# Performance work log

Measured on AMD Instinct MI355X. Metric: run time of the kernel, lower is better.

Reference implementation:

```python
import jax, jax.numpy as jnp
import numpy as np

B, S, D = 2, 2048, 1024
H, DK = 16, 64  # n_heads, d_kv; inner_dim = H*DK = D


def setup_inputs() -> dict:
    key = jax.random.key(0)
    ks = jax.random.split(key, 7)
    scale = 1.0 / np.sqrt(D)
    return {
        "hidden_states": jax.random.normal(ks[0], (B, S, D), dtype=jnp.float32),
        "position_bias": jax.random.normal(ks[1], (1, H, S, S), dtype=jnp.float32) * 0.1,
        "key_value_states": jax.random.normal(ks[2], (B, S, D), dtype=jnp.float32),
        "wq": jax.random.normal(ks[3], (D, H * DK), dtype=jnp.float32) * scale,
        "wk": jax.random.normal(ks[4], (D, H * DK), dtype=jnp.float32) * scale,
        "wv": jax.random.normal(ks[5], (D, H * DK), dtype=jnp.float32) * scale,
        "wo": jax.random.normal(ks[6], (H * DK, D), dtype=jnp.float32) * scale,
    }


def reference(hidden_states, position_bias, key_value_states, wq, wk, wv, wo):
    # Self-attention branch (is_cross_attention=False): K/V come from hidden_states.
    b, s, _ = hidden_states.shape
    kv_src = hidden_states  # would be key_value_states if cross-attention

    def split_heads(x):  # [b, s, H*DK] -> [b, H, s, DK]
        return x.reshape(b, -1, H, DK).transpose(0, 2, 1, 3)

    q = split_heads(hidden_states @ wq)
    k = split_heads(kv_src @ wk)
    v = split_heads(kv_src @ wv)

    # T5-style: NO 1/sqrt(d_k) scaling; additive position bias.
    scores = jnp.einsum("bhqd,bhkd->bhqk", q, k) + position_bias
    attn = jax.nn.softmax(scores.astype(jnp.float32), axis=-1).astype(scores.dtype)
    ctx = jnp.einsum("bhqk,bhkd->bhqd", attn, v)
    ctx = ctx.transpose(0, 2, 1, 3).reshape(b, s, H * DK)
    return ctx @ wo
```

## Files before the change

kernel.cpp:

```cpp
#include <hip/hip_runtime.h>
#include <math.h>

#define B_  2
#define S_  2048
#define D_  1024
#define H_  16
#define DK_ 64

typedef float f32x4 __attribute__((ext_vector_type(4)));
typedef short short8 __attribute__((ext_vector_type(8)));
typedef unsigned short u16;

static __device__ __forceinline__ u16 f2bf(float x) {
    union { float f; unsigned u; } v; v.f = x;
    unsigned r = v.u + 0x7fffu + ((v.u >> 16) & 1u);
    return (u16)(r >> 16);
}

static __device__ __forceinline__ void gload_lds16(const void* g, void* l) {
    __builtin_amdgcn_global_load_lds((const __attribute__((address_space(1))) void*)g,
                                     (__attribute__((address_space(3))) void*)l,
                                     16, 0, 0);
}

#define MFMA16(a, b, c) __builtin_amdgcn_mfma_f32_16x16x32_bf16((a), (b), (c), 0, 0, 0)

__global__ __launch_bounds__(256) void cast_bf16(const float* __restrict__ X,
                                                 u16* __restrict__ Y) {
    int i = (blockIdx.x * 256 + threadIdx.x) * 8;
    float4 a = *(const float4*)(X + i);
    float4 b = *(const float4*)(X + i + 4);
    short8 o;
    o[0] = (short)f2bf(a.x); o[1] = (short)f2bf(a.y);
    o[2] = (short)f2bf(a.z); o[3] = (short)f2bf(a.w);
    o[4] = (short)f2bf(b.x); o[5] = (short)f2bf(b.y);
    o[6] = (short)f2bf(b.z); o[7] = (short)f2bf(b.w);
    *(short8*)(Y + i) = o;
}

__global__ __launch_bounds__(256) void transpose_cast4(const float* __restrict__ w0,
                                                       const float* __restrict__ w1,
                                                       const float* __restrict__ w2,
                                                       const float* __restrict__ w3,
                                                       u16* __restrict__ o0,
                                                       u16* __restrict__ o1,
                                                       u16* __restrict__ o2,
                                                       u16* __restrict__ o3) {
    __shared__ float t[32][33];
    const float* W; u16* O;
    switch (blockIdx.z) {
        case 0: W = w0; O = o0; break;
        case 1: W = w1; O = o1; break;
        case 2: W = w2; O = o2; break;
        default: W = w3; O = o3; break;
    }
    const int K = 1024, N = 1024;
    int tx = threadIdx.x & 31, ty = threadIdx.x >> 5;
    int n0 = blockIdx.x * 32, k0 = blockIdx.y * 32;
#pragma unroll
    for (int r = ty; r < 32; r += 8)
        t[r][tx] = W[(size_t)(k0 + r) * N + n0 + tx];
    __syncthreads();
#pragma unroll
    for (int r = ty; r < 32; r += 8)
        O[(size_t)(n0 + r) * K + k0 + tx] = f2bf(t[tx][r]);
}

template <int MODE>
__global__ __launch_bounds__(256) void gemm_bf16(const u16* __restrict__ A,
                                                 const u16* __restrict__ Bt,
                                                 void* __restrict__ C0,
                                                 u16* __restrict__ Kb,
                                                 u16* __restrict__ Vt,
                                                 int M, int N, int K) {
    __shared__ alignas(16) u16 As[128 * 32];
    __shared__ alignas(16) u16 Bs[128 * 32];

    const int tid  = threadIdx.x;
    const int wave = tid >> 6;
    const int lane = tid & 63;
    const int col  = lane & 15;
    const int quad = lane >> 4;
    const int bm   = blockIdx.y * 128;
    const int bn   = blockIdx.x * 128;
    const int wm   = (wave >> 1) * 64;
    const int wn   = (wave & 1) * 64;

    f32x4 acc[4][4];
#pragma unroll
    for (int i = 0; i < 4; ++i)
#pragma unroll
        for (int j = 0; j < 4; ++j) acc[i][j] = (f32x4){0.f, 0.f, 0.f, 0.f};

    const int srow = wave * 32 + (lane >> 2);
    const int ksel = (lane & 3) * 8;
    const u16* ga0 = A  + (size_t)(bm + srow) * K + ksel;
    const u16* ga1 = ga0 + (size_t)16 * K;
    const u16* gb0 = Bt + (size_t)(bn + srow) * K + ksel;
    const u16* gb1 = gb0 + (size_t)16 * K;
    char* la0 = (char*)As + wave * 2048;
    char* la1 = la0 + 1024;
    char* lb0 = (char*)Bs + wave * 2048;
    char* lb1 = lb0 + 1024;

    for (int k0 = 0; k0 < K; k0 += 32) {
        __syncthreads();
        gload_lds16(ga0 + k0, la0);
        gload_lds16(ga1 + k0, la1);
        gload_lds16(gb0 + k0, lb0);
        gload_lds16(gb1 + k0, lb1);
        __syncthreads();
        short8 af[4], bfr[4];
#pragma unroll
        for (int mi = 0; mi < 4; ++mi)
            af[mi] = *(const short8*)&As[(wm + mi * 16 + col) * 32 + quad * 8];
#pragma unroll
        for (int ni = 0; ni < 4; ++ni)
            bfr[ni] = *(const short8*)&Bs[(wn + ni * 16 + col) * 32 + quad * 8];
#pragma unroll
        for (int mi = 0; mi < 4; ++mi)
#pragma unroll
            for (int ni = 0; ni < 4; ++ni)
                acc[mi][ni] = MFMA16(af[mi], bfr[ni], acc[mi][ni]);
    }

#pragma unroll
    for (int mi = 0; mi < 4; ++mi)
#pragma unroll
        for (int ni = 0; ni < 4; ++ni) {
            const int rowb = bm + wm + mi * 16 + quad * 4;
            const int coln = bn + wn + ni * 16 + col;
            f32x4 v = acc[mi][ni];
            if (MODE == 2) {
                float* O = (float*)C0;
#pragma unroll
                for (int r = 0; r < 4; ++r)
                    O[(size_t)(rowb + r) * N + coln] = v[r];
            } else {
                if (coln < D_) {
                    u16* Qb = (u16*)C0;
#pragma unroll
                    for (int r = 0; r < 4; ++r)
                        Qb[(size_t)(rowb + r) * D_ + coln] = f2bf(v[r]);
                } else if (coln < 2 * D_) {
#pragma unroll
                    for (int r = 0; r < 4; ++r)
                        Kb[(size_t)(rowb + r) * D_ + (coln - D_)] = f2bf(v[r]);
                } else {
                    const int nn = coln - 2 * D_;
                    const int hh = nn >> 6, d = nn & 63;
                    const int bb = rowb >> 11, sb = rowb & 2047;
                    ushort4 pk;
                    pk.x = f2bf(v[0]); pk.y = f2bf(v[1]);
                    pk.z = f2bf(v[2]); pk.w = f2bf(v[3]);
                    *(ushort4*)&Vt[(((size_t)bb * H_ + hh) * DK_ + d) * S_ + sb] = pk;
                }
            }
        }
}

__global__ __launch_bounds__(256, 4) void attn_mfma(const u16* __restrict__ Qb,
                                                    const u16* __restrict__ Kb,
                                                    const u16* __restrict__ Vt,
                                                    const float* __restrict__ bias,
                                                    u16* __restrict__ Ctx) {
    __shared__ alignas(16) char smem[40960];

    const int tid  = threadIdx.x;
    const int wave = tid >> 6;
    const int lane = tid & 63;
    const int col  = lane & 15;
    const int quad = lane >> 4;
    const int cx   = col & 7;
    const int sl0  = (quad ^ cx) * 16;
    const int sl1  = ((4 + quad) ^ cx) * 16;

    const int gid = blockIdx.x;
    const int qt  = gid & 31;
    const int h   = (gid >> 5) & 15;
    const int b   = gid >> 9;
    const int q0  = qt * 64 + wave * 16;

    short8 aq0, aq1;
    {
        const u16* qp = Qb + (size_t)(b * S_ + q0 + col) * D_ + h * 64 + quad * 8;
        aq0 = *(const short8*)qp;
        aq1 = *(const short8*)(qp + 32);
    }

    const int c0 = tid, c1 = tid + 256;
    const int r0 = c0 >> 3, g0 = (c0 & 7) ^ (r0 & 7);
    const int r1 = c1 >> 3, g1 = (c1 & 7) ^ (r1 & 7);
    const u16* kT = Kb + (size_t)b * S_ * D_ + h * 64;
    const u16* vT = Vt + ((size_t)b * H_ + h) * (size_t)64 * S_;
    const size_t kOff0 = (size_t)r0 * D_ + g0 * 8;
    const size_t kOff1 = (size_t)r1 * D_ + g1 * 8;
    const size_t vOff0 = (size_t)r0 * S_ + g0 * 8;
    const size_t vOff1 = (size_t)r1 * S_ + g1 * 8;

    auto stage = [&](int j0s, int bis) {
        char* base = smem + bis * 16384;
        gload_lds16(kT + (size_t)j0s * D_ + kOff0, base + wave * 1024);
        gload_lds16(kT + (size_t)j0s * D_ + kOff1, base + 4096 + wave * 1024);
        gload_lds16(vT + j0s + vOff0, base + 8192 + wave * 1024);
        gload_lds16(vT + j0s + vOff1, base + 12288 + wave * 1024);
    };

    f32x4 o[4];
#pragma unroll
    for (int i = 0; i < 4; ++i) o[i] = (f32x4){0.f, 0.f, 0.f, 0.f};
    float mst[4], lst[4];
#pragma unroll
    for (int r = 0; r < 4; ++r) { mst[r] = -INFINITY; lst[r] = 0.f; }

    const float* bias_base = bias + ((size_t)h * S_ + (q0 + quad * 4)) * S_;
    char* pw = smem + 32768 + wave * 2048;

    stage(0, 0);

    for (int it = 0; it < 32; ++it) {
        const int j0 = it * 64;
        const int bi = it & 1;
        __syncthreads();
        if (it < 31) stage(j0 + 64, bi ^ 1);

        const char* bK = smem + bi * 16384;
        const char* bV = bK + 8192;

        float bb[16];
#pragma unroll
        for (int ng = 0; ng < 4; ++ng)
#pragma unroll
            for (int r = 0; r < 4; ++r)
                bb[ng * 4 + r] = bias_base[(size_t)r * S_ + j0 + ng * 16 + col];

        f32x4 sc[4];
#pragma unroll
        for (int ng = 0; ng < 4; ++ng) {
            const char* rp = bK + (ng * 16 + col) * 128;
            short8 k0 = *(const short8*)(rp + sl0);
            short8 k1 = *(const short8*)(rp + sl1);
            f32x4 z = (f32x4){0.f, 0.f, 0.f, 0.f};
            z = MFMA16(aq0, k0, z);
            z = MFMA16(aq1, k1, z);
            sc[ng] = z;
        }
#pragma unroll
        for (int ng = 0; ng < 4; ++ng)
#pragma unroll
            for (int r = 0; r < 4; ++r) sc[ng][r] += bb[ng * 4 + r];

        float alpha[4], rs[4];
#pragma unroll
        for (int r = 0; r < 4; ++r) {
            float rm = fmaxf(fmaxf(sc[0][r], sc[1][r]), fmaxf(sc[2][r], sc[3][r]));
            rm = fmaxf(rm, __shfl_xor(rm, 1));
            rm = fmaxf(rm, __shfl_xor(rm, 2));
            rm = fmaxf(rm, __shfl_xor(rm, 4));
            rm = fmaxf(rm, __shfl_xor(rm, 8));
            float mn = fmaxf(mst[r], rm);
            alpha[r] = __expf(mst[r] - mn);
            mst[r] = mn;
            rs[r] = 0.f;
        }
#pragma unroll
        for (int ng = 0; ng < 4; ++ng)
#pragma unroll
            for (int r = 0; r < 4; ++r) {
                float p = __expf(sc[ng][r] - mst[r]);
                sc[ng][r] = p;
                rs[r] += p;
            }
#pragma unroll
        for (int r = 0; r < 4; ++r) {
            float s = rs[r];
            s += __shfl_xor(s, 1);
            s += __shfl_xor(s, 2);
            s += __shfl_xor(s, 4);
            s += __shfl_xor(s, 8);
            lst[r] = lst[r] * alpha[r] + s;
        }
#pragma unroll
        for (int ndg = 0; ndg < 4; ++ndg)
#pragma unroll
            for (int r = 0; r < 4; ++r) o[ndg][r] *= alpha[r];

#pragma unroll
        for (int ng = 0; ng < 4; ++ng) {
            const int cb = ng * 2 + (col >> 3);
#pragma unroll
            for (int r = 0; r < 4; ++r) {
                const int q = quad * 4 + r;
                *(u16*)(pw + q * 128 + ((cb ^ (q & 7)) * 16) + cx * 2) = f2bf(sc[ng][r]);
            }
        }
        short8 ap0 = *(const short8*)(pw + col * 128 + sl0);
        short8 ap1 = *(const short8*)(pw + col * 128 + sl1);

#pragma unroll
        for (int ndg = 0; ndg < 4; ++ndg) {
            const char* rp = bV + (ndg * 16 + col) * 128;
            short8 v0 = *(const short8*)(rp + sl0);
            short8 v1 = *(const short8*)(rp + sl1);
            o[ndg] = MFMA16(ap0, v0, o[ndg]);
            o[ndg] = MFMA16(ap1, v1, o[ndg]);
        }
    }

    float inv[4];
#pragma unroll
    for (int r = 0; r < 4; ++r) inv[r] = 1.f / lst[r];
#pragma unroll
    for (int ndg = 0; ndg < 4; ++ndg)
#pragma unroll
        for (int r = 0; r < 4; ++r)
            Ctx[(size_t)(b * S_ + q0 + quad * 4 + r) * D_ + h * 64 + ndg * 16 + col] =
                f2bf(o[ndg][r] * inv[r]);
}

extern "C" void kernel_launch(void* const* d_in, const int* in_sizes, int n_in,
                              void* d_out, int out_size, void* d_ws, size_t ws_size,
                              hipStream_t stream) {
    const float* hs   = (const float*)d_in[0];
    const float* bias = (const float*)d_in[1];
    const float* wq   = (const float*)d_in[3];
    const float* wk   = (const float*)d_in[4];
    const float* wv   = (const float*)d_in[5];
    const float* wo   = (const float*)d_in[6];
    float* out = (float*)d_out;

    const size_t elems = (size_t)B_ * S_ * D_;
    char* ws = (char*)d_ws;
    u16* hs_bf = (u16*)ws;
    u16* qb    = (u16*)(ws + 8 * 1024 * 1024);
    u16* kb    = (u16*)(ws + 16 * 1024 * 1024);
    u16* vt    = (u16*)(ws + 24 * 1024 * 1024);
    u16* cb    = (u16*)(ws + 32 * 1024 * 1024);
    u16* wqt   = (u16*)(ws + 40 * 1024 * 1024);
    u16* wkt   = (u16*)(ws + 42 * 1024 * 1024);
    u16* wvt   = (u16*)(ws + 44 * 1024 * 1024);
    u16* wot   = (u16*)(ws + 46 * 1024 * 1024);

    const int M = B_ * S_;

    cast_bf16<<<(int)(elems / (256 * 8)), 256, 0, stream>>>(hs, hs_bf);
    transpose_cast4<<<dim3(32, 32, 4), 256, 0, stream>>>(wq, wk, wv, wo,
                                                         wqt, wkt, wvt, wot);

    gemm_bf16<0><<<dim3(3 * D_ / 128, M / 128), 256, 0, stream>>>(
        hs_bf, wqt, (void*)qb, kb, vt, M, 3 * D_, D_);

    attn_mfma<<<B_ * H_ * (S_ / 64), 256, 0, stream>>>(qb, kb, vt, bias, cb);

    gemm_bf16<2><<<dim3(D_ / 128, M / 128), 256, 0, stream>>>(
        cb, wot, (void*)out, nullptr, nullptr, M, D_, D_);
}
```

Measured before the change: 528.6 us.

## Double-buffer GEMM LDS tiles and merge cast and transpose prep kernels

The bf16 GEMM now keeps two LDS buffers for A and B. The next k-slice's global-to-LDS load is issued right after the barrier, while the current slice feeds the MFMAs, and the second barrier per iteration is gone. It also adds a launch-bounds occupancy hint of 2. Separately, the hidden-state cast and the weight transpose-cast are merged into one launch, using an extra grid z-slice, to save a kernel launch. The cost is doubled LDS use per block, which could limit occupancy.

```diff
diff --git a/kernel.cpp b/kernel.cpp
--- a/kernel.cpp
+++ b/kernel.cpp
@@ -25,27 +25,31 @@
 
 #define MFMA16(a, b, c) __builtin_amdgcn_mfma_f32_16x16x32_bf16((a), (b), (c), 0, 0, 0)
 
-__global__ __launch_bounds__(256) void cast_bf16(const float* __restrict__ X,
-                                                 u16* __restrict__ Y) {
-    int i = (blockIdx.x * 256 + threadIdx.x) * 8;
-    float4 a = *(const float4*)(X + i);
-    float4 b = *(const float4*)(X + i + 4);
-    short8 o;
-    o[0] = (short)f2bf(a.x); o[1] = (short)f2bf(a.y);
-    o[2] = (short)f2bf(a.z); o[3] = (short)f2bf(a.w);
-    o[4] = (short)f2bf(b.x); o[5] = (short)f2bf(b.y);
-    o[6] = (short)f2bf(b.z); o[7] = (short)f2bf(b.w);
-    *(short8*)(Y + i) = o;
-}
-
-__global__ __launch_bounds__(256) void transpose_cast4(const float* __restrict__ w0,
-                                                       const float* __restrict__ w1,
-                                                       const float* __restrict__ w2,
-                                                       const float* __restrict__ w3,
-                                                       u16* __restrict__ o0,
-                                                       u16* __restrict__ o1,
-                                                       u16* __restrict__ o2,
-                                                       u16* __restrict__ o3) {
+__global__ __launch_bounds__(256) void prep(const float* __restrict__ hs,
+                                            const float* __restrict__ w0,
+                                            const float* __restrict__ w1,
+                                            const float* __restrict__ w2,
+                                            const float* __restrict__ w3,
+                                            u16* __restrict__ hsb,
+                                            u16* __restrict__ o0,
+                                            u16* __restrict__ o1,
+                                            u16* __restrict__ o2,
+                                            u16* __restrict__ o3) {
+    if (blockIdx.z == 4) {
+        size_t i = ((size_t)(blockIdx.y * 32 + blockIdx.x) * 256 + threadIdx.x) * 16;
+#pragma unroll
+        for (int c = 0; c < 2; ++c) {
+            float4 a = *(const float4*)(hs + i + c * 8);
+            float4 b = *(const float4*)(hs + i + c * 8 + 4);
+            short8 o;
+            o[0] = (short)f2bf(a.x); o[1] = (short)f2bf(a.y);
+            o[2] = (short)f2bf(a.z); o[3] = (short)f2bf(a.w);
+            o[4] = (short)f2bf(b.x); o[5] = (short)f2bf(b.y);
+            o[6] = (short)f2bf(b.z); o[7] = (short)f2bf(b.w);
+            *(short8*)(hsb + i + c * 8) = o;
+        }
+        return;
+    }
     __shared__ float t[32][33];
     const float* W; u16* O;
     switch (blockIdx.z) {
@@ -67,14 +71,14 @@
 }
 
 template <int MODE>
-__global__ __launch_bounds__(256) void gemm_bf16(const u16* __restrict__ A,
-                                                 const u16* __restrict__ Bt,
-                                                 void* __restrict__ C0,
-                                                 u16* __restrict__ Kb,
-                                                 u16* __restrict__ Vt,
-                                                 int M, int N, int K) {
-    __shared__ alignas(16) u16 As[128 * 32];
-    __shared__ alignas(16) u16 Bs[128 * 32];
+__global__ __launch_bounds__(256, 2) void gemm_bf16(const u16* __restrict__ A,
+                                                    const u16* __restrict__ Bt,
+                                                    void* __restrict__ C0,
+                                                    u16* __restrict__ Kb,
+                                                    u16* __restrict__ Vt,
+                                                    int M, int N, int K) {
+    __shared__ alignas(16) u16 As[2][128 * 32];
+    __shared__ alignas(16) u16 Bs[2][128 * 32];
 
     const int tid  = threadIdx.x;
     const int wave = tid >> 6;
@@ -94,29 +98,36 @@
 
     const int srow = wave * 32 + (lane >> 2);
     const int ksel = (lane & 3) * 8;
-    const u16* ga0 = A  + (size_t)(bm + srow) * K + ksel;
-    const u16* ga1 = ga0 + (size_t)16 * K;
-    const u16* gb0 = Bt + (size_t)(bn + srow) * K + ksel;
-    const u16* gb1 = gb0 + (size_t)16 * K;
-    char* la0 = (char*)As + wave * 2048;
-    char* la1 = la0 + 1024;
-    char* lb0 = (char*)Bs + wave * 2048;
-    char* lb1 = lb0 + 1024;
-
-    for (int k0 = 0; k0 < K; k0 += 32) {
+    const u16* gA = A  + (size_t)(bm + srow) * K + ksel;
+    const u16* gB = Bt + (size_t)(bn + srow) * K + ksel;
+    const size_t rowJump = (size_t)16 * K;
+    const int ldsOff = wave * 2048;
+
+    auto stage = [&](int k0, int bi) {
+        char* a = (char*)As[bi] + ldsOff;
+        char* b = (char*)Bs[bi] + ldsOff;
+        gload_lds16(gA + k0, a);
+        gload_lds16(gA + k0 + rowJump, a + 1024);
+        gload_lds16(gB + k0, b);
+        gload_lds16(gB + k0 + rowJump, b + 1024);
+    };
+
+    stage(0, 0);
+    const int NIT = K >> 5;
+    for (int it = 0; it < NIT; ++it) {
+        const int bi = it & 1;
         __syncthreads();
-        gload_lds16(ga0 + k0, la0);
-        gload_lds16(ga1 + k0, la1);
-        gload_lds16(gb0 + k0, lb0);
-        gload_lds16(gb1 + k0, lb1);
-        __syncthreads();
+        if (it + 1 < NIT) stage((it + 1) * 32, bi ^ 1);
+
+        const u16* as = As[bi];
+        const u16* bs = Bs[bi];
         short8 af[4], bfr[4];
 #pragma unroll
         for (int mi = 0; mi < 4; ++mi)
-            af[mi] = *(const short8*)&As[(wm + mi * 16 + col) * 32 + quad * 8];
+            af[mi] = *(const short8*)&as[(wm + mi * 16 + col) * 32 + quad * 8];
 #pragma unroll
         for (int ni = 0; ni < 4; ++ni)
-            bfr[ni] = *(const short8*)&Bs[(wn + ni * 16 + col) * 32 + quad * 8];
+            bfr[ni] = *(const short8*)&bs[(wn + ni * 16 + col) * 32 + quad * 8];
 #pragma unroll
         for (int mi = 0; mi < 4; ++mi)
 #pragma unroll
@@ -329,7 +340,6 @@
     const float* wo   = (const float*)d_in[6];
     float* out = (float*)d_out;
 
-    const size_t elems = (size_t)B_ * S_ * D_;
     char* ws = (char*)d_ws;
     u16* hs_bf = (u16*)ws;
     u16* qb    = (u16*)(ws + 8 * 1024 * 1024);
@@ -343,9 +353,8 @@
 
     const int M = B_ * S_;
 
-    cast_bf16<<<(int)(elems / (256 * 8)), 256, 0, stream>>>(hs, hs_bf);
-    transpose_cast4<<<dim3(32, 32, 4), 256, 0, stream>>>(wq, wk, wv, wo,
-                                                         wqt, wkt, wvt, wot);
+    prep<<<dim3(32, 32, 5), 256, 0, stream>>>(hs, wq, wk, wv, wo,
+                                              hs_bf, wqt, wkt, wvt, wot);
 
     gemm_bf16<0><<<dim3(3 * D_ / 128, M / 128), 256, 0, stream>>>(
         hs_bf, wqt, (void*)qb, kb, vt, M, 3 * D_, D_);
```

After: 522.3 us. No clear change (-1.2%).
